# Kernel optimization log

Measured on AMD Instinct MI355X. Metric: run time of the kernel, lower is better.

The kernel has to match this reference:

```python
import jax, jax.numpy as jnp
import numpy as np

T, B, D, H = 1024, 32, 512, 512
EPS = 1e-5


def _lstm_dir(gates_x, w_hh, reverse):
    # gates_x: [T, B, 4H] = x @ W_ih^T + b_ih + b_hh (precomputed)
    Hh = w_hh.shape[1]

    def step(carry, g):
        h, c = carry
        gates = g + h @ w_hh.T  # [B, 4H]
        i, f, gg, o = jnp.split(gates, 4, axis=-1)  # torch gate order i,f,g,o
        i = jax.nn.sigmoid(i)
        f = jax.nn.sigmoid(f)
        gg = jnp.tanh(gg)
        o = jax.nn.sigmoid(o)
        c = f * c + i * gg
        h = o * jnp.tanh(c)
        return (h, c), h

    Bc = gates_x.shape[1]
    init = (jnp.zeros((Bc, Hh), gates_x.dtype), jnp.zeros((Bc, Hh), gates_x.dtype))
    _, hs = jax.lax.scan(step, init, gates_x, reverse=reverse)
    return hs  # [T, B, H], time-aligned with input


def setup_inputs() -> dict:
    key = jax.random.key(0)
    ks = jax.random.split(key, 10)
    s = 1.0 / np.sqrt(H)
    inp = {
        "x": jax.random.normal(ks[0], (T, B, D), jnp.float32),
        "gamma": jnp.ones((D,), jnp.float32),
        "beta": jnp.zeros((D,), jnp.float32),
        "w_ih_f": jax.random.uniform(ks[1], (4 * H, D), jnp.float32, -s, s),
        "w_hh_f": jax.random.uniform(ks[2], (4 * H, H), jnp.float32, -s, s),
        "b_ih_f": jax.random.uniform(ks[3], (4 * H,), jnp.float32, -s, s),
        "b_hh_f": jax.random.uniform(ks[4], (4 * H,), jnp.float32, -s, s),
        "w_ih_b": jax.random.uniform(ks[5], (4 * H, D), jnp.float32, -s, s),
        "w_hh_b": jax.random.uniform(ks[6], (4 * H, H), jnp.float32, -s, s),
        "b_ih_b": jax.random.uniform(ks[7], (4 * H,), jnp.float32, -s, s),
        "b_hh_b": jax.random.uniform(ks[8], (4 * H,), jnp.float32, -s, s),
    }
    return inp


def reference(x, gamma, beta, w_ih_f, w_hh_f, b_ih_f, b_hh_f, w_ih_b, w_hh_b, b_ih_b, b_hh_b):
    # LayerNorm over last dim
    mu = jnp.mean(x, axis=-1, keepdims=True)
    var = jnp.mean(jnp.square(x - mu), axis=-1, keepdims=True)
    xn = (x - mu) * jax.lax.rsqrt(var + EPS) * gamma + beta
    # Precompute input-to-hidden gates for both directions
    gx_f = jnp.einsum('tbd,gd->tbg', xn, w_ih_f) + b_ih_f + b_hh_f
    gx_b = jnp.einsum('tbd,gd->tbg', xn, w_ih_b) + b_ih_b + b_hh_b
    h_f = _lstm_dir(gx_f, w_hh_f, reverse=False)
    h_b = _lstm_dir(gx_b, w_hh_b, reverse=True)
    # concat(fwd, bwd) -> view(T,B,2,H).sum(2) == elementwise sum of directions
    return h_f + h_b
```

## Files before the change

kernel.cpp:

```cpp
#include <hip/hip_runtime.h>
#include <hip/hip_bf16.h>

#define T_LEN 1024
#define NB    32
#define DD    512
#define HH    512
#define EPS_  1e-5f

typedef unsigned short u16;
typedef unsigned int   u32;
typedef unsigned long long u64;
typedef float  f32x16 __attribute__((ext_vector_type(16)));
typedef short  bf16x8 __attribute__((ext_vector_type(8)));

__device__ __forceinline__ u16 f2bf(float f) {
    union { float f; u32 u; } cv; cv.f = f;
    u32 r = cv.u + 0x7FFFu + ((cv.u >> 16) & 1u);
    return (u16)(r >> 16);
}
__device__ __forceinline__ float fsig(float x) {
    return 1.0f / (1.0f + __expf(-x));
}
__device__ __forceinline__ float ftanh(float x) {
    float ax = fabsf(x);
    float e  = __expf(-2.0f * ax);
    float t  = (1.0f - e) / (1.0f + e);
    return copysignf(t, x);
}
__device__ __forceinline__ int lds_load(int* p) {
    return __hip_atomic_load(p, __ATOMIC_ACQUIRE, __HIP_MEMORY_SCOPE_WORKGROUP);
}
__device__ __forceinline__ void lds_add_release(int* p) {
    __hip_atomic_fetch_add(p, 1, __ATOMIC_RELEASE, __HIP_MEMORY_SCOPE_WORKGROUP);
}

__global__ __launch_bounds__(256) void ln_kernel(const float* __restrict__ x,
                                                 const float* __restrict__ gamma,
                                                 const float* __restrict__ beta,
                                                 u16* __restrict__ xn) {
    int wave = threadIdx.x >> 6, lane = threadIdx.x & 63;
    long row = (long)blockIdx.x * 4 + wave;
    const float* xr = x + row * DD;
    int c0 = lane * 8;
    float4 v0 = *(const float4*)(xr + c0);
    float4 v1 = *(const float4*)(xr + c0 + 4);
    float s = v0.x+v0.y+v0.z+v0.w + v1.x+v1.y+v1.z+v1.w;
    float q = v0.x*v0.x+v0.y*v0.y+v0.z*v0.z+v0.w*v0.w
            + v1.x*v1.x+v1.y*v1.y+v1.z*v1.z+v1.w*v1.w;
    #pragma unroll
    for (int m = 1; m < 64; m <<= 1) { s += __shfl_xor(s, m); q += __shfl_xor(q, m); }
    float mu  = s * (1.0f / DD);
    float var = q * (1.0f / DD) - mu * mu;
    float rs  = rsqrtf(var + EPS_);
    float4 g0 = *(const float4*)(gamma + c0), g1 = *(const float4*)(gamma + c0 + 4);
    float4 b0 = *(const float4*)(beta  + c0), b1 = *(const float4*)(beta  + c0 + 4);
    float o[8];
    o[0]=(v0.x-mu)*rs*g0.x+b0.x; o[1]=(v0.y-mu)*rs*g0.y+b0.y;
    o[2]=(v0.z-mu)*rs*g0.z+b0.z; o[3]=(v0.w-mu)*rs*g0.w+b0.w;
    o[4]=(v1.x-mu)*rs*g1.x+b1.x; o[5]=(v1.y-mu)*rs*g1.y+b1.y;
    o[6]=(v1.z-mu)*rs*g1.z+b1.z; o[7]=(v1.w-mu)*rs*g1.w+b1.w;
    uint4 pk;
    pk.x = (u32)f2bf(o[0]) | ((u32)f2bf(o[1]) << 16);
    pk.y = (u32)f2bf(o[2]) | ((u32)f2bf(o[3]) << 16);
    pk.z = (u32)f2bf(o[4]) | ((u32)f2bf(o[5]) << 16);
    pk.w = (u32)f2bf(o[6]) | ((u32)f2bf(o[7]) << 16);
    *(uint4*)(xn + row * DD + c0) = pk;
}

__global__ __launch_bounds__(256) void prep_kernel(
        const float* __restrict__ wih_f, const float* __restrict__ whh_f,
        const float* __restrict__ bih_f, const float* __restrict__ bhh_f,
        const float* __restrict__ wih_b, const float* __restrict__ whh_b,
        const float* __restrict__ bih_b, const float* __restrict__ bhh_b,
        u16* __restrict__ Wc, float* __restrict__ biasC,
        u64* __restrict__ data, int* __restrict__ sent) {
    long i0 = (long)blockIdx.x * 256 + threadIdx.x;
    long stride = (long)gridDim.x * 256;
    for (long idx = i0; idx < 4194304L; idx += stride) {
        int m = (int)(idx >> 20); int off = (int)(idx & 1048575L);
        const float* src = (m == 0) ? wih_f : (m == 1) ? whh_f : (m == 2) ? wih_b : whh_b;
        Wc[idx] = f2bf(src[off]);
        if (idx < 4096L) {
            int d = (int)(idx >> 11), n = (int)(idx & 2047L);
            biasC[idx] = d ? (bih_b[n] + bhh_b[n]) : (bih_f[n] + bhh_f[n]);
        }
        if (idx < 16384L) data[idx] = 0;
        if (idx < 128L)   sent[idx] = -1;
    }
}

__global__ __launch_bounds__(256) void add_kernel(float* __restrict__ out,
                                                  const u16* __restrict__ hist) {
    long i0 = (long)blockIdx.x * 256 + threadIdx.x;
    long stride = (long)gridDim.x * 256;
    const ushort4* h4 = (const ushort4*)hist;
    float4* o4 = (float4*)out;
    for (long i = i0; i < 4194304L; i += stride) {
        float4 o = o4[i];
        ushort4 h = h4[i];
        o.x += __uint_as_float((u32)h.x << 16);
        o.y += __uint_as_float((u32)h.y << 16);
        o.z += __uint_as_float((u32)h.z << 16);
        o.w += __uint_as_float((u32)h.w << 16);
        o4[i] = o;
    }
}

#define SMEM_BYTES 98432
__global__ __launch_bounds__(512) void scan_kernel(
        const u16* __restrict__ xn, const u16* __restrict__ Wc,
        const float* __restrict__ biasC, u64* __restrict__ data,
        int* __restrict__ sent, float* __restrict__ out, u16* __restrict__ hist) {
    extern __shared__ char smem_raw[];
    u16*   xn_lds = (u16*)smem_raw;
    u16*   h_lds  = xn_lds + 16384;
    float* accx   = (float*)(h_lds + 16384);
    int*   ctr    = (int*)(accx + 8192);

    const int wg   = blockIdx.x & 15;
    const int dir  = blockIdx.x >> 4;
    const int w    = threadIdx.x >> 6;
    const int lane = threadIdx.x & 63;
    const bool is_x = (w < 4);
    const int g    = w & 3;
    const int bcol = lane & 31;
    const int hi   = lane >> 5;
    const int hi8  = hi * 8;
    const int swz  = (bcol & 7) << 3;
    const int tid4 = (w & 3) * 64 + lane;

    bf16x8 afrag[32];
    {
        int rowA = lane & 31;
        const u16* Wm = Wc + (size_t)(dir * 2 + (is_x ? 0 : 1)) * (2048 * 512)
                      + (size_t)((rowA >> 3) * 512 + wg * 32 + g * 8 + (rowA & 7)) * 512 + hi8;
        #pragma unroll 32
        for (int kc = 0; kc < 32; kc++) afrag[kc] = *(const bf16x8*)(Wm + kc * 16);
    }
    float bias_r[16];
    if (is_x) {
        #pragma unroll 16
        for (int r = 0; r < 16; r++)
            bias_r[r] = biasC[dir * 2048 + (r >> 2) * 512 + wg * 32 + g * 8 + (r & 3) + 4 * hi];
    }
    if (threadIdx.x == 0) {
        ctr[0] = 0; ctr[1] = 0; ctr[2] = 0; ctr[3] = 0; ctr[4] = -1;
    }
    __syncthreads();

    if (is_x) {
        bf16x8 xpre[8];
        {
            const u16* src = xn + (size_t)(dir ? (T_LEN - 1) : 0) * (NB * DD);
            #pragma unroll 8
            for (int r = 0; r < 8; r++)
                xpre[r] = *(const bf16x8*)(src + (tid4 + 256 * r) * 8);
        }
        int kbar = 0;
        #pragma unroll 1
        for (int i = 0; i < T_LEN; ++i) {
            if (i >= 2) {
                long gg = 2000000000L;
                while (lds_load(&ctr[3]) < 4 * (i - 1) && --gg > 0) {}
            }
            if (lane == 0) lds_add_release(&ctr[0]);
            kbar++;
            { long gg = 2000000000L;
              while (lds_load(&ctr[0]) < 4 * kbar && --gg > 0) {} }
            #pragma unroll 8
            for (int r = 0; r < 8; r++) {
                int u = (tid4 + 256 * r) * 8;
                int b = u >> 9, cu = u & 511;
                *(bf16x8*)(xn_lds + b * 512 + (cu ^ ((b & 7) << 3))) = xpre[r];
            }
            if (lane == 0) lds_add_release(&ctr[0]);
            kbar++;
            { long gg = 2000000000L;
              while (lds_load(&ctr[0]) < 4 * kbar && --gg > 0) {} }
            if (i + 1 < T_LEN) {
                const u16* src = xn + (size_t)(dir ? (T_LEN - 2 - i) : (i + 1)) * (NB * DD);
                #pragma unroll 8
                for (int r = 0; r < 8; r++)
                    xpre[r] = *(const bf16x8*)(src + (tid4 + 256 * r) * 8);
            }
            f32x16 a0, a1;
            #pragma unroll 16
            for (int r = 0; r < 16; r++) { a0[r] = 0.f; a1[r] = 0.f; }
            #pragma unroll 16
            for (int k2 = 0; k2 < 16; k2++) {
                bf16x8 b0 = *(const bf16x8*)(xn_lds + bcol * 512 + (((2*k2  )*16 + hi8) ^ swz));
                bf16x8 b1 = *(const bf16x8*)(xn_lds + bcol * 512 + (((2*k2+1)*16 + hi8) ^ swz));
                a0 = __builtin_amdgcn_mfma_f32_32x32x16_bf16(afrag[2*k2],   b0, a0, 0, 0, 0);
                a1 = __builtin_amdgcn_mfma_f32_32x32x16_bf16(afrag[2*k2+1], b1, a1, 0, 0, 0);
            }
            float* dst = accx + (i & 1) * 4096 + g * 1024;
            #pragma unroll 16
            for (int r = 0; r < 16; r++) dst[r * 64 + lane] = a0[r] + a1[r] + bias_r[r];
            if (lane == 0) lds_add_release(&ctr[1]);
        }
    } else {
        float c_st[4] = {0.f, 0.f, 0.f, 0.f};
        #pragma unroll 8
        for (int k = 0; k < 8; k++)
            *(uint4*)(h_lds + tid4 * 64 + k * 8) = uint4{0, 0, 0, 0};
        int kh = 0;
        if (lane == 0) lds_add_release(&ctr[2]);
        kh++;
        { long gg = 2000000000L;
          while (lds_load(&ctr[2]) < 4 * kh && --gg > 0) {} }

        #pragma unroll 1
        for (int sg = 0; sg < T_LEN; ++sg) {
            if (sg >= 1) {
                if (g == 0) {
                    const int* sp = sent + dir * 64 + lane;
                    int guard = 600000;
                    while (true) {
                        int v = __hip_atomic_load(sp, __ATOMIC_RELAXED,
                                                  __HIP_MEMORY_SCOPE_AGENT);
                        if (__all(v >= sg - 1) || --guard == 0) break;
                        __builtin_amdgcn_s_sleep(1);
                    }
                    __hip_atomic_store(&ctr[4], sg - 1, __ATOMIC_RELEASE,
                                       __HIP_MEMORY_SCOPE_WORKGROUP);
                } else {
                    long gg = 2000000000L;
                    while (__hip_atomic_load(&ctr[4], __ATOMIC_ACQUIRE,
                                             __HIP_MEMORY_SCOPE_WORKGROUP) < sg - 1
                           && --gg > 0) {}
                }
                const char* bp = (const char*)(data + (size_t)(dir * 2 + ((sg - 1) & 1)) * 4096)
                               + (size_t)tid4 * 16;
                uint4 dq[8];
                #pragma unroll 8
                for (int n = 0; n < 8; n++) {
                    const char* ap = bp + n * 4096;
                    uint4 v;
                    asm volatile("global_load_dwordx4 %0, %1, off sc0 sc1"
                                 : "=&v"(v) : "v"(ap));
                    dq[n] = v;
                }
                asm volatile("s_waitcnt vmcnt(0)" ::: "memory");
                __builtin_amdgcn_sched_barrier(0);
                int b  = tid4 & 31;
                int qh = tid4 >> 5;
                int sw = (b & 7) << 3;
                u16* hr = h_lds + b * 512;
                #pragma unroll 8
                for (int n = 0; n < 8; n++) {
                    int j = 64 * n + 8 * qh;
                    *(bf16x8*)(hr + (j ^ sw)) = *(const bf16x8*)&dq[n];
                }
                if (lane == 0) lds_add_release(&ctr[2]);
                kh++;
                { long gg = 2000000000L;
                  while (lds_load(&ctr[2]) < 4 * kh && --gg > 0) {} }
            }
            f32x16 a0, a1;
            #pragma unroll 16
            for (int r = 0; r < 16; r++) { a0[r] = 0.f; a1[r] = 0.f; }
            if (sg >= 1) {
                #pragma unroll 16
                for (int k2 = 0; k2 < 16; k2++) {
                    bf16x8 b0 = *(const bf16x8*)(h_lds + bcol * 512 + (((2*k2  )*16 + hi8) ^ swz));
                    bf16x8 b1 = *(const bf16x8*)(h_lds + bcol * 512 + (((2*k2+1)*16 + hi8) ^ swz));
                    a0 = __builtin_amdgcn_mfma_f32_32x32x16_bf16(afrag[2*k2],   b0, a0, 0, 0, 0);
                    a1 = __builtin_amdgcn_mfma_f32_32x32x16_bf16(afrag[2*k2+1], b1, a1, 0, 0, 0);
                }
            }
            { long gg = 2000000000L;
              while (lds_load(&ctr[1]) < 4 * (sg + 1) && --gg > 0) {} }
            const float* ax = accx + (sg & 1) * 4096 + g * 1024;
            float hv[4];
            #pragma unroll 4
            for (int m = 0; m < 4; m++) {
                float gi = a0[m]      + a1[m]      + ax[(m     ) * 64 + lane];
                float gf = a0[4 + m]  + a1[4 + m]  + ax[(4 + m ) * 64 + lane];
                float gg_= a0[8 + m]  + a1[8 + m]  + ax[(8 + m ) * 64 + lane];
                float go = a0[12 + m] + a1[12 + m] + ax[(12 + m) * 64 + lane];
                float ig = fsig(gi), fg = fsig(gf), gv = ftanh(gg_), og = fsig(go);
                float c = fg * c_st[m] + ig * gv;
                c_st[m] = c;
                hv[m] = og * ftanh(c);
            }
            if (lane == 0) lds_add_release(&ctr[3]);
            u64 pk = (u64)f2bf(hv[0]) | ((u64)f2bf(hv[1]) << 16)
                   | ((u64)f2bf(hv[2]) << 32) | ((u64)f2bf(hv[3]) << 48);
            if (sg < T_LEN - 1) {
                u64* dp = data + (size_t)(dir * 2 + (sg & 1)) * 4096
                        + (size_t)((wg * 4 + g) * 64 + bcol * 2 + hi);
                __hip_atomic_store(dp, pk, __ATOMIC_RELAXED, __HIP_MEMORY_SCOPE_AGENT);
                asm volatile("s_waitcnt vmcnt(0)" ::: "memory");
                if (lane == 0)
                    __hip_atomic_store(sent + dir * 64 + wg * 4 + g, sg,
                                       __ATOMIC_RELAXED, __HIP_MEMORY_SCOPE_AGENT);
            }
            int tph = dir ? (T_LEN - 1 - sg) : sg;
            int jq  = wg * 32 + g * 8 + 4 * hi;
            if (dir == 0) {
                float4 o4v = make_float4(hv[0], hv[1], hv[2], hv[3]);
                *(float4*)(out + ((size_t)tph * NB + bcol) * HH + jq) = o4v;
            } else {
                *(u64*)(hist + ((size_t)tph * NB + bcol) * HH + jq) = pk;
            }
        }
    }
}

extern "C" void kernel_launch(void* const* d_in, const int* in_sizes, int n_in,
                              void* d_out, int out_size, void* d_ws, size_t ws_size,
                              hipStream_t stream) {
    const float* x     = (const float*)d_in[0];
    const float* gamma = (const float*)d_in[1];
    const float* beta  = (const float*)d_in[2];
    const float* wih_f = (const float*)d_in[3];
    const float* whh_f = (const float*)d_in[4];
    const float* bih_f = (const float*)d_in[5];
    const float* bhh_f = (const float*)d_in[6];
    const float* wih_b = (const float*)d_in[7];
    const float* whh_b = (const float*)d_in[8];
    const float* bih_b = (const float*)d_in[9];
    const float* bhh_b = (const float*)d_in[10];
    float* out = (float*)d_out;

    u16*   xn    = (u16*)d_ws;
    u16*   Wc    = xn + 16777216;
    float* biasC = (float*)(Wc + 4194304);
    u64*   data  = (u64*)(biasC + 4096);
    int*   sent  = (int*)(data + 16384);
    u16*   hist  = (u16*)(sent + 128);

    (void)hipFuncSetAttribute((const void*)scan_kernel,
                              hipFuncAttributeMaxDynamicSharedMemorySize, SMEM_BYTES);

    ln_kernel<<<dim3(8192), dim3(256), 0, stream>>>(x, gamma, beta, xn);
    prep_kernel<<<dim3(4096), dim3(256), 0, stream>>>(wih_f, whh_f, bih_f, bhh_f,
                                                      wih_b, whh_b, bih_b, bhh_b,
                                                      Wc, biasC, data, sent);
    scan_kernel<<<dim3(32), dim3(512), SMEM_BYTES, stream>>>(xn, Wc, biasC, data,
                                                             sent, out, hist);
    add_kernel<<<dim3(2048), dim3(256), 0, stream>>>(out, hist);
}
```

Baseline: 4.767 ms.

## Halve scan workgroups to 8 per direction with 1024 threads each

The persistent scan kernel now runs 8 workgroups per direction, each with 16 waves (8 input-projection and 8 recurrent), instead of 16 workgroups with 8 waves. Each workgroup publishes a single aggregated sentinel after all its recurrent waves have stored h, tracked through a new LDS counter. Pollers therefore watch 8 flags instead of 64, and they spin a few rounds before sleeping. The aim is to cut the cross-workgroup synchronisation cost on every timestep. In exchange, each workgroup uses more LDS and a larger intra-workgroup barrier, and sentinel publication is serialised through the last wave to finish.

```diff
diff --git a/kernel.cpp b/kernel.cpp
--- a/kernel.cpp
+++ b/kernel.cpp
@@ -30,8 +30,8 @@
 __device__ __forceinline__ int lds_load(int* p) {
     return __hip_atomic_load(p, __ATOMIC_ACQUIRE, __HIP_MEMORY_SCOPE_WORKGROUP);
 }
-__device__ __forceinline__ void lds_add_release(int* p) {
-    __hip_atomic_fetch_add(p, 1, __ATOMIC_RELEASE, __HIP_MEMORY_SCOPE_WORKGROUP);
+__device__ __forceinline__ int lds_add_release(int* p) {
+    return __hip_atomic_fetch_add(p, 1, __ATOMIC_RELEASE, __HIP_MEMORY_SCOPE_WORKGROUP);
 }
 
 __global__ __launch_bounds__(256) void ln_kernel(const float* __restrict__ x,
@@ -106,8 +106,8 @@
     }
 }
 
-#define SMEM_BYTES 98432
-__global__ __launch_bounds__(512) void scan_kernel(
+#define SMEM_BYTES 131104
+__global__ __launch_bounds__(1024) void scan_kernel(
         const u16* __restrict__ xn, const u16* __restrict__ Wc,
         const float* __restrict__ biasC, u64* __restrict__ data,
         int* __restrict__ sent, float* __restrict__ out, u16* __restrict__ hist) {
@@ -115,25 +115,26 @@
     u16*   xn_lds = (u16*)smem_raw;
     u16*   h_lds  = xn_lds + 16384;
     float* accx   = (float*)(h_lds + 16384);
-    int*   ctr    = (int*)(accx + 8192);
-
-    const int wg   = blockIdx.x & 15;
-    const int dir  = blockIdx.x >> 4;
+    int*   ctr    = (int*)(accx + 16384);
+
+    const int wg2  = blockIdx.x & 7;
+    const int dir  = blockIdx.x >> 3;
     const int w    = threadIdx.x >> 6;
     const int lane = threadIdx.x & 63;
-    const bool is_x = (w < 4);
-    const int g    = w & 3;
+    const bool is_x = (w < 8);
+    const int gw   = w & 7;
+    const int C3   = wg2 * 8 + gw;
     const int bcol = lane & 31;
     const int hi   = lane >> 5;
     const int hi8  = hi * 8;
     const int swz  = (bcol & 7) << 3;
-    const int tid4 = (w & 3) * 64 + lane;
+    const int tid8 = gw * 64 + lane;
 
     bf16x8 afrag[32];
     {
         int rowA = lane & 31;
         const u16* Wm = Wc + (size_t)(dir * 2 + (is_x ? 0 : 1)) * (2048 * 512)
-                      + (size_t)((rowA >> 3) * 512 + wg * 32 + g * 8 + (rowA & 7)) * 512 + hi8;
+                      + (size_t)((rowA >> 3) * 512 + C3 * 8 + (rowA & 7)) * 512 + hi8;
         #pragma unroll 32
         for (int kc = 0; kc < 32; kc++) afrag[kc] = *(const bf16x8*)(Wm + kc * 16);
     }
@@ -141,47 +142,47 @@
     if (is_x) {
         #pragma unroll 16
         for (int r = 0; r < 16; r++)
-            bias_r[r] = biasC[dir * 2048 + (r >> 2) * 512 + wg * 32 + g * 8 + (r & 3) + 4 * hi];
+            bias_r[r] = biasC[dir * 2048 + (r >> 2) * 512 + C3 * 8 + (r & 3) + 4 * hi];
     }
     if (threadIdx.x == 0) {
-        ctr[0] = 0; ctr[1] = 0; ctr[2] = 0; ctr[3] = 0; ctr[4] = -1;
+        ctr[0] = 0; ctr[1] = 0; ctr[2] = 0; ctr[3] = 0; ctr[4] = -1; ctr[5] = 0;
     }
     __syncthreads();
 
     if (is_x) {
-        bf16x8 xpre[8];
+        bf16x8 xpre[4];
         {
             const u16* src = xn + (size_t)(dir ? (T_LEN - 1) : 0) * (NB * DD);
-            #pragma unroll 8
-            for (int r = 0; r < 8; r++)
-                xpre[r] = *(const bf16x8*)(src + (tid4 + 256 * r) * 8);
+            #pragma unroll 4
+            for (int r = 0; r < 4; r++)
+                xpre[r] = *(const bf16x8*)(src + (tid8 + 512 * r) * 8);
         }
         int kbar = 0;
         #pragma unroll 1
         for (int i = 0; i < T_LEN; ++i) {
             if (i >= 2) {
                 long gg = 2000000000L;
-                while (lds_load(&ctr[3]) < 4 * (i - 1) && --gg > 0) {}
-            }
-            if (lane == 0) lds_add_release(&ctr[0]);
+                while (lds_load(&ctr[3]) < 8 * (i - 1) && --gg > 0) {}
+            }
+            if (lane == 0) (void)lds_add_release(&ctr[0]);
             kbar++;
             { long gg = 2000000000L;
-              while (lds_load(&ctr[0]) < 4 * kbar && --gg > 0) {} }
-            #pragma unroll 8
-            for (int r = 0; r < 8; r++) {
-                int u = (tid4 + 256 * r) * 8;
+              while (lds_load(&ctr[0]) < 8 * kbar && --gg > 0) {} }
+            #pragma unroll 4
+            for (int r = 0; r < 4; r++) {
+                int u = (tid8 + 512 * r) * 8;
                 int b = u >> 9, cu = u & 511;
                 *(bf16x8*)(xn_lds + b * 512 + (cu ^ ((b & 7) << 3))) = xpre[r];
             }
-            if (lane == 0) lds_add_release(&ctr[0]);
+            if (lane == 0) (void)lds_add_release(&ctr[0]);
             kbar++;
             { long gg = 2000000000L;
-              while (lds_load(&ctr[0]) < 4 * kbar && --gg > 0) {} }
+              while (lds_load(&ctr[0]) < 8 * kbar && --gg > 0) {} }
             if (i + 1 < T_LEN) {
                 const u16* src = xn + (size_t)(dir ? (T_LEN - 2 - i) : (i + 1)) * (NB * DD);
-                #pragma unroll 8
-                for (int r = 0; r < 8; r++)
-                    xpre[r] = *(const bf16x8*)(src + (tid4 + 256 * r) * 8);
+                #pragma unroll 4
+                for (int r = 0; r < 4; r++)
+                    xpre[r] = *(const bf16x8*)(src + (tid8 + 512 * r) * 8);
             }
             f32x16 a0, a1;
             #pragma unroll 16
@@ -193,33 +194,33 @@
                 a0 = __builtin_amdgcn_mfma_f32_32x32x16_bf16(afrag[2*k2],   b0, a0, 0, 0, 0);
                 a1 = __builtin_amdgcn_mfma_f32_32x32x16_bf16(afrag[2*k2+1], b1, a1, 0, 0, 0);
             }
-            float* dst = accx + (i & 1) * 4096 + g * 1024;
+            float* dst = accx + (i & 1) * 8192 + gw * 1024;
             #pragma unroll 16
             for (int r = 0; r < 16; r++) dst[r * 64 + lane] = a0[r] + a1[r] + bias_r[r];
-            if (lane == 0) lds_add_release(&ctr[1]);
+            if (lane == 0) (void)lds_add_release(&ctr[1]);
         }
     } else {
         float c_st[4] = {0.f, 0.f, 0.f, 0.f};
-        #pragma unroll 8
-        for (int k = 0; k < 8; k++)
-            *(uint4*)(h_lds + tid4 * 64 + k * 8) = uint4{0, 0, 0, 0};
+        #pragma unroll 4
+        for (int k = 0; k < 4; k++)
+            *(uint4*)(h_lds + tid8 * 32 + k * 8) = uint4{0, 0, 0, 0};
         int kh = 0;
-        if (lane == 0) lds_add_release(&ctr[2]);
+        if (lane == 0) (void)lds_add_release(&ctr[2]);
         kh++;
         { long gg = 2000000000L;
-          while (lds_load(&ctr[2]) < 4 * kh && --gg > 0) {} }
+          while (lds_load(&ctr[2]) < 8 * kh && --gg > 0) {} }
 
         #pragma unroll 1
         for (int sg = 0; sg < T_LEN; ++sg) {
             if (sg >= 1) {
-                if (g == 0) {
-                    const int* sp = sent + dir * 64 + lane;
-                    int guard = 600000;
+                if (gw == 0) {
+                    const int* sp = sent + dir * 8 + (lane & 7);
+                    int rounds = 0, guard = 600000;
                     while (true) {
                         int v = __hip_atomic_load(sp, __ATOMIC_RELAXED,
                                                   __HIP_MEMORY_SCOPE_AGENT);
                         if (__all(v >= sg - 1) || --guard == 0) break;
-                        __builtin_amdgcn_s_sleep(1);
+                        if (++rounds > 4) __builtin_amdgcn_s_sleep(1);
                     }
                     __hip_atomic_store(&ctr[4], sg - 1, __ATOMIC_RELEASE,
                                        __HIP_MEMORY_SCOPE_WORKGROUP);
@@ -230,11 +231,11 @@
                            && --gg > 0) {}
                 }
                 const char* bp = (const char*)(data + (size_t)(dir * 2 + ((sg - 1) & 1)) * 4096)
-                               + (size_t)tid4 * 16;
-                uint4 dq[8];
-                #pragma unroll 8
-                for (int n = 0; n < 8; n++) {
-                    const char* ap = bp + n * 4096;
+                               + (size_t)tid8 * 16;
+                uint4 dq[4];
+                #pragma unroll 4
+                for (int n = 0; n < 4; n++) {
+                    const char* ap = bp + n * 8192;
                     uint4 v;
                     asm volatile("global_load_dwordx4 %0, %1, off sc0 sc1"
                                  : "=&v"(v) : "v"(ap));
@@ -242,19 +243,19 @@
                 }
                 asm volatile("s_waitcnt vmcnt(0)" ::: "memory");
                 __builtin_amdgcn_sched_barrier(0);
-                int b  = tid4 & 31;
-                int qh = tid4 >> 5;
+                int b  = tid8 & 31;
+                int q  = tid8 >> 5;
                 int sw = (b & 7) << 3;
                 u16* hr = h_lds + b * 512;
-                #pragma unroll 8
-                for (int n = 0; n < 8; n++) {
-                    int j = 64 * n + 8 * qh;
+                #pragma unroll 4
+                for (int n = 0; n < 4; n++) {
+                    int j = (q + 16 * n) * 8;
                     *(bf16x8*)(hr + (j ^ sw)) = *(const bf16x8*)&dq[n];
                 }
-                if (lane == 0) lds_add_release(&ctr[2]);
+                if (lane == 0) (void)lds_add_release(&ctr[2]);
                 kh++;
                 { long gg = 2000000000L;
-                  while (lds_load(&ctr[2]) < 4 * kh && --gg > 0) {} }
+                  while (lds_load(&ctr[2]) < 8 * kh && --gg > 0) {} }
             }
             f32x16 a0, a1;
             #pragma unroll 16
@@ -269,8 +270,8 @@
                 }
             }
             { long gg = 2000000000L;
-              while (lds_load(&ctr[1]) < 4 * (sg + 1) && --gg > 0) {} }
-            const float* ax = accx + (sg & 1) * 4096 + g * 1024;
+              while (lds_load(&ctr[1]) < 8 * (sg + 1) && --gg > 0) {} }
+            const float* ax = accx + (sg & 1) * 8192 + gw * 1024;
             float hv[4];
             #pragma unroll 4
             for (int m = 0; m < 4; m++) {
@@ -283,20 +284,23 @@
                 c_st[m] = c;
                 hv[m] = og * ftanh(c);
             }
-            if (lane == 0) lds_add_release(&ctr[3]);
+            if (lane == 0) (void)lds_add_release(&ctr[3]);
             u64 pk = (u64)f2bf(hv[0]) | ((u64)f2bf(hv[1]) << 16)
                    | ((u64)f2bf(hv[2]) << 32) | ((u64)f2bf(hv[3]) << 48);
             if (sg < T_LEN - 1) {
                 u64* dp = data + (size_t)(dir * 2 + (sg & 1)) * 4096
-                        + (size_t)((wg * 4 + g) * 64 + bcol * 2 + hi);
+                        + (size_t)(C3 * 64 + bcol * 2 + hi);
                 __hip_atomic_store(dp, pk, __ATOMIC_RELAXED, __HIP_MEMORY_SCOPE_AGENT);
                 asm volatile("s_waitcnt vmcnt(0)" ::: "memory");
-                if (lane == 0)
-                    __hip_atomic_store(sent + dir * 64 + wg * 4 + g, sg,
-                                       __ATOMIC_RELAXED, __HIP_MEMORY_SCOPE_AGENT);
+                if (lane == 0) {
+                    int prev = lds_add_release(&ctr[5]);
+                    if ((prev & 7) == 7)
+                        __hip_atomic_store(sent + dir * 8 + wg2, sg,
+                                           __ATOMIC_RELAXED, __HIP_MEMORY_SCOPE_AGENT);
+                }
             }
             int tph = dir ? (T_LEN - 1 - sg) : sg;
-            int jq  = wg * 32 + g * 8 + 4 * hi;
+            int jq  = C3 * 8 + 4 * hi;
             if (dir == 0) {
                 float4 o4v = make_float4(hv[0], hv[1], hv[2], hv[3]);
                 *(float4*)(out + ((size_t)tph * NB + bcol) * HH + jq) = o4v;
@@ -337,7 +341,7 @@
     prep_kernel<<<dim3(4096), dim3(256), 0, stream>>>(wih_f, whh_f, bih_f, bhh_f,
                                                       wih_b, whh_b, bih_b, bhh_b,
                                                       Wc, biasC, data, sent);
-    scan_kernel<<<dim3(32), dim3(512), SMEM_BYTES, stream>>>(xn, Wc, biasC, data,
-                                                             sent, out, hist);
+    scan_kernel<<<dim3(16), dim3(1024), SMEM_BYTES, stream>>>(xn, Wc, biasC, data,
+                                                              sent, out, hist);
     add_kernel<<<dim3(2048), dim3(256), 0, stream>>>(out, hist);
 }
```

Measured after the change: 14.89 ms. 3.12x slower.
